# Performance work log

Measured on AMD Instinct MI355X. Metric: run time of the kernel, lower is better.

## Reference

```python
import jax, jax.numpy as jnp
import numpy as np

B, L, HID, NH = 8, 1024, 1024, 16
DH = HID // NH
EPS = 1e-12


def _linear(x, W, b):
    # torch nn.Linear: y = x @ W.T + b
    return jnp.einsum('ble,oe->blo', x, W) + b


def _attend(qx, kx, vx, mask, Wq, bq, Wk, bk, Wv, bv):
    q = _linear(qx, Wq, bq).reshape(B, -1, NH, DH)
    k = _linear(kx, Wk, bk).reshape(B, -1, NH, DH)
    v = _linear(vx, Wv, bv).reshape(B, -1, NH, DH)
    scores = jnp.einsum('bqhd,bkhd->bhqk', q, k) / np.sqrt(DH).astype(np.float32)
    scores = scores + mask  # additive mask broadcast [B,1,1,Lk]
    probs = jax.nn.softmax(scores, axis=-1)  # dropout = identity (eval mode)
    ctx = jnp.einsum('bhqk,bkhd->bqhd', probs, v)
    return ctx.reshape(B, -1, HID)


def _layernorm(x, gamma, beta):
    mu = jnp.mean(x, axis=-1, keepdims=True)
    var = jnp.mean(jnp.square(x - mu), axis=-1, keepdims=True)
    return gamma * (x - mu) * jax.lax.rsqrt(var + EPS) + beta


def setup_inputs():
    key = jax.random.key(0)
    ks = jax.random.split(key, 20)
    s = 0.02
    d = {
        'cinput_tensor': jax.random.normal(ks[0], (B, L, HID), jnp.float32),
        'qinput_tensor': jax.random.normal(ks[1], (B, L, HID), jnp.float32),
        'attention_mask': jnp.zeros((B, 1, 1, L), jnp.float32),
        'qattention_mask': jnp.zeros((B, 1, 1, L), jnp.float32),
    }
    names = ['Wq', 'Wk', 'Wv', 'Wqq', 'Wqk', 'Wqv', 'Wo']
    for i, n in enumerate(names):
        d[n] = jax.random.normal(ks[2 + i], (HID, HID), jnp.float32) * s
        d['b' + n[1:]] = jnp.zeros((HID,), jnp.float32)
    d['gamma'] = jnp.ones((HID,), jnp.float32)
    d['beta'] = jnp.zeros((HID,), jnp.float32)
    return d


def reference(cinput_tensor, qinput_tensor, attention_mask, qattention_mask,
              Wq, bq, Wk, bk, Wv, bv, Wqq, bqq, Wqk, bqk, Wqv, bqv,
              Wo, bo, gamma, beta):
    enc, dec = cinput_tensor, qinput_tensor
    # c-branch: query from dec, key/value from enc
    ctx = _attend(dec, enc, enc, attention_mask, Wq, bq, Wk, bk, Wv, bv)
    # q-branch: query from enc, key/value from dec
    qctx = _attend(enc, dec, dec, qattention_mask, Wqq, bqq, Wqk, bqk, Wqv, bqv)
    # output: same dense/LayerNorm reused, and BOTH residuals add cinput_tensor
    # (faithful to the original module, including its apparent bug)
    c_out = _layernorm(_linear(ctx, Wo, bo) + cinput_tensor, gamma, beta)
    q_out = _layernorm(_linear(qctx, Wo, bo) + cinput_tensor, gamma, beta)
    return (c_out, q_out)
```

## Files before the change

kernel.cpp:

```cpp
#include <hip/hip_runtime.h>

typedef __bf16 bf16;
typedef unsigned short u16;
typedef __bf16 bf16x8 __attribute__((ext_vector_type(8)));
typedef __bf16 bf16x4 __attribute__((ext_vector_type(4)));
typedef float f32x4 __attribute__((ext_vector_type(4)));

#define GLD16(g, l) __builtin_amdgcn_global_load_lds( \
    (const __attribute__((address_space(1))) void*)(g), \
    (__attribute__((address_space(3))) void*)(l), 16, 0, 0)

#define MFMA_BF16 __builtin_amdgcn_mfma_f32_16x16x32_bf16

#define FENCE() asm volatile("" ::: "memory")
#define BARRIER() do { FENCE(); __builtin_amdgcn_s_barrier(); FENCE(); } while (0)

struct CvtFlat { const float* s[9]; bf16* d[9]; int off[10]; };

__global__ __launch_bounds__(256) void cvt_flat(CvtFlat a) {
  const int g = blockIdx.x * 256 + threadIdx.x;
  int seg = 0;
  #pragma unroll
  for (int i = 1; i < 9; ++i) seg += (g >= a.off[i]) ? 1 : 0;
  const int loc = (g - a.off[seg]) * 4;
  const f32x4 v = *(const f32x4*)(a.s[seg] + loc);
  bf16x4 o;
  #pragma unroll
  for (int j = 0; j < 4; ++j) o[j] = (bf16)v[j];
  *(bf16x4*)(a.d[seg] + loc) = o;
}

struct GemmDesc {
  const bf16* X;
  const bf16* W;
  const float* B;
  const float* R;
  bf16* Y;
  int vt;
};
struct GemmArgs { GemmDesc d[6]; };

__device__ __forceinline__ void stage_slice(const bf16* G, int row0, int k0,
                                            u16* slot, int w, int lane) {
  #pragma unroll
  for (int i = 0; i < 2; ++i) {
    const int sb = i * 512 + w * 64;
    const int s = sb + lane;
    const int r = s >> 2, c = (s & 3) ^ ((r >> 1) & 3);
    GLD16(G + (row0 + r) * 1024 + k0 + c * 8, &slot[sb * 8]);
  }
}

template <bool STAGE, int VW>
__device__ __forceinline__ void do_slice(
    int sv, u16 (&As)[4][8192], u16 (&Bs)[4][8192], f32x4 (&acc)[8][4],
    const int (&offA)[8], const int (&offB)[4],
    const bf16* __restrict__ X, const bf16* __restrict__ W,
    int m0, int n0, int w, int lane) {
  const u16* Asl = &As[sv & 3][0];
  const u16* Bsl = &Bs[sv & 3][0];
  bf16x8 a[4], b[4];
  #pragma unroll
  for (int mt = 0; mt < 4; ++mt) a[mt] = *(const bf16x8*)&Asl[offA[mt]];
  #pragma unroll
  for (int nt = 0; nt < 4; ++nt) b[nt] = *(const bf16x8*)&Bsl[offB[nt]];
  if constexpr (STAGE)
    stage_slice(X, m0, (sv + 3) * 32, &As[(sv + 3) & 3][0], w, lane);
  BARRIER();
  asm volatile("s_waitcnt lgkmcnt(0)" ::: "memory");
  __builtin_amdgcn_s_setprio(1);
  #pragma unroll
  for (int mt = 0; mt < 4; ++mt)
    #pragma unroll
    for (int nt = 0; nt < 4; ++nt)
      acc[mt][nt] = MFMA_BF16(a[mt], b[nt], acc[mt][nt], 0, 0, 0);
  __builtin_amdgcn_s_setprio(0);
  BARRIER();
  #pragma unroll
  for (int mt = 0; mt < 4; ++mt) a[mt] = *(const bf16x8*)&Asl[offA[4 + mt]];
  if constexpr (STAGE)
    stage_slice(W, n0, (sv + 3) * 32, &Bs[(sv + 3) & 3][0], w, lane);
  BARRIER();
  asm volatile("s_waitcnt lgkmcnt(0)" ::: "memory");
  __builtin_amdgcn_s_setprio(1);
  #pragma unroll
  for (int mt = 0; mt < 4; ++mt)
    #pragma unroll
    for (int nt = 0; nt < 4; ++nt)
      acc[4 + mt][nt] = MFMA_BF16(a[mt], b[nt], acc[4 + mt][nt], 0, 0, 0);
  __builtin_amdgcn_s_setprio(0);
  if constexpr (VW == 8)      asm volatile("s_waitcnt vmcnt(8)" ::: "memory");
  else if constexpr (VW == 4) asm volatile("s_waitcnt vmcnt(4)" ::: "memory");
  else if constexpr (VW == 0) asm volatile("s_waitcnt vmcnt(0)" ::: "memory");
  BARRIER();
}

__global__ __launch_bounds__(512, 2) void gemm256(GemmArgs args) {
  const GemmDesc g = args.d[blockIdx.z];
  __shared__ u16 As[4][8192];
  __shared__ u16 Bs[4][8192];
  const int tid = threadIdx.x;
  const int w = tid >> 6, lane = tid & 63;
  const int lq = lane >> 4, ll = lane & 15;
  const int wr = w >> 2, wc = w & 3;
  const int lin = blockIdx.x + (blockIdx.y << 3);
  const int tile = (lin & 7) * 16 + (lin >> 3);
  const int mtile = tile >> 2, ntile = tile & 3;
  const int m0 = mtile * 256, n0 = ntile * 256;
  f32x4 acc[8][4] = {};

  int offA[8], offB[4];
  #pragma unroll
  for (int mt = 0; mt < 8; ++mt) {
    const int am = wr * 128 + mt * 16 + ll;
    offA[mt] = (am * 4 + (lq ^ ((am >> 1) & 3))) * 8;
  }
  #pragma unroll
  for (int nt = 0; nt < 4; ++nt) {
    const int bn = wc * 64 + nt * 16 + ll;
    offB[nt] = (bn * 4 + (lq ^ ((bn >> 1) & 3))) * 8;
  }

  #pragma unroll
  for (int ss = 0; ss < 3; ++ss) {
    stage_slice(g.X, m0, ss * 32, &As[ss][0], w, lane);
    stage_slice(g.W, n0, ss * 32, &Bs[ss][0], w, lane);
  }
  asm volatile("s_waitcnt vmcnt(8)" ::: "memory");
  BARRIER();

  #pragma unroll 4
  for (int s = 0; s < 28; ++s)
    do_slice<true, 8>(s, As, Bs, acc, offA, offB, g.X, g.W, m0, n0, w, lane);
  do_slice<true, 8>(28, As, Bs, acc, offA, offB, g.X, g.W, m0, n0, w, lane);
  do_slice<false, 4>(29, As, Bs, acc, offA, offB, g.X, g.W, m0, n0, w, lane);
  do_slice<false, 0>(30, As, Bs, acc, offA, offB, g.X, g.W, m0, n0, w, lane);
  do_slice<false, -1>(31, As, Bs, acc, offA, offB, g.X, g.W, m0, n0, w, lane);

  float biasv[4];
  #pragma unroll
  for (int nt = 0; nt < 4; ++nt) biasv[nt] = g.B[n0 + wc * 64 + nt * 16 + ll];

  #pragma unroll
  for (int mt = 0; mt < 8; ++mt) {
    #pragma unroll
    for (int r = 0; r < 4; ++r) {
      const int m = m0 + wr * 128 + mt * 16 + lq * 4 + r;
      #pragma unroll
      for (int nt = 0; nt < 4; ++nt) {
        const int n = n0 + wc * 64 + nt * 16 + ll;
        float v = acc[mt][nt][r] + biasv[nt];
        if (g.R) v += g.R[m * 1024 + n];
        if (!g.vt) {
          g.Y[m * 1024 + n] = (bf16)v;
        } else {
          const int bb = m >> 10, tok = m & 1023;
          g.Y[(((bb << 4) + (n >> 6)) * 64 + (n & 63)) * 1024 + tok] = (bf16)v;
        }
      }
    }
  }
}

struct AttnDesc { const bf16* Qp; const bf16* Kp; const bf16* Vt; const float* mask; bf16* ctx; };

__global__ __launch_bounds__(256, 4) void attn_kernel(AttnDesc A0, AttnDesc A1) {
  const AttnDesc A = blockIdx.z ? A1 : A0;
  __shared__ u16 Ks[128 * 64];
  __shared__ u16 Vts[64 * 128];
  __shared__ u16 Pts[4 * 1024];
  const int tid = threadIdx.x;
  const int w = tid >> 6, lane = tid & 63;
  const int lq = lane >> 4, ll = lane & 15;
  const int lin = blockIdx.x + (blockIdx.y << 3);
  const int bh = (lin & 7) | ((lin >> 6) << 3);
  const int q0 = ((lin >> 3) & 7) * 128;
  const int b = bh >> 4, h = bh & 15;
  const float* mrow = A.mask + b * 1024;

  #pragma unroll
  for (int i = 0; i < 4; ++i) {
    const int sb = w * 256 + i * 64;
    const int s = sb + lane;
    const int r = s >> 3, c = (s & 7) ^ (r & 7);
    GLD16(A.Qp + (b * 1024 + q0 + r) * 1024 + h * 64 + c * 8, &Ks[sb * 8]);
  }
  __syncthreads();
  bf16x8 bq[2][2];
  #pragma unroll
  for (int nt = 0; nt < 2; ++nt)
    #pragma unroll
    for (int kd = 0; kd < 2; ++kd) {
      const int row = w * 32 + nt * 16 + ll;
      const int c8 = kd * 4 + lq;
      bq[nt][kd] = *(const bf16x8*)&Ks[row * 64 + ((c8 ^ (row & 7)) << 3)];
    }
  __syncthreads();

  f32x4 oacc[4][2] = {};
  float rsum[2] = {0.f, 0.f};

  for (int kt = 0; kt < 8; ++kt) {
    const int kk0 = kt * 128;
    #pragma unroll
    for (int i = 0; i < 4; ++i) {
      const int sb = w * 256 + i * 64;
      const int s = sb + lane;
      { const int r = s >> 3, c = (s & 7) ^ (r & 7);
        GLD16(A.Kp + (b * 1024 + kk0 + r) * 1024 + h * 64 + c * 8, &Ks[sb * 8]); }
      { const int r = s >> 4, c = (s & 15) ^ (r & 15);
        GLD16(A.Vt + (bh * 64 + r) * 1024 + kk0 + c * 8, &Vts[sb * 8]); }
    }
    __syncthreads();

    #pragma unroll
    for (int qtr = 0; qtr < 4; ++qtr) {
      bf16x8 ak[2][2];
      #pragma unroll
      for (int mh = 0; mh < 2; ++mh) {
        const int row = qtr * 32 + mh * 16 + ll;
        #pragma unroll
        for (int kd = 0; kd < 2; ++kd) {
          const int c8 = kd * 4 + lq;
          ak[mh][kd] = *(const bf16x8*)&Ks[row * 64 + ((c8 ^ (row & 7)) << 3)];
        }
      }
      f32x4 sacc[2][2] = {};
      #pragma unroll
      for (int mh = 0; mh < 2; ++mh)
        #pragma unroll
        for (int nt = 0; nt < 2; ++nt)
          #pragma unroll
          for (int kd = 0; kd < 2; ++kd)
            sacc[mh][nt] = MFMA_BF16(ak[mh][kd], bq[nt][kd], sacc[mh][nt], 0, 0, 0);

      f32x4 mv[2];
      #pragma unroll
      for (int mh = 0; mh < 2; ++mh)
        mv[mh] = *(const f32x4*)&mrow[kk0 + qtr * 32 + mh * 16 + lq * 4];

      #pragma unroll
      for (int mh = 0; mh < 2; ++mh)
        #pragma unroll
        for (int nt = 0; nt < 2; ++nt) {
          bf16x4 pv;
          #pragma unroll
          for (int rr = 0; rr < 4; ++rr) {
            const float p = __expf(fmaf(sacc[mh][nt][rr], 0.125f, mv[mh][rr]));
            rsum[nt] += p;
            pv[rr] = (bf16)p;
          }
          const int row = nt * 16 + ll;
          const int gq = mh * 2 + (lq >> 1);
          *(bf16x4*)&Pts[w * 1024 + row * 32 + ((gq ^ (row & 3)) << 3) + (lq & 1) * 4] = pv;
        }

      bf16x8 bp[2];
      #pragma unroll
      for (int nt = 0; nt < 2; ++nt) {
        const int row = nt * 16 + ll;
        bp[nt] = *(const bf16x8*)&Pts[w * 1024 + row * 32 + ((lq ^ (row & 3)) << 3)];
      }
      #pragma unroll
      for (int mtd = 0; mtd < 4; ++mtd) {
        const int row = mtd * 16 + ll;
        const int c16 = (qtr * 4 + lq) ^ (row & 15);
        const bf16x8 av = *(const bf16x8*)&Vts[row * 128 + (c16 << 3)];
        oacc[mtd][0] = MFMA_BF16(av, bp[0], oacc[mtd][0], 0, 0, 0);
        oacc[mtd][1] = MFMA_BF16(av, bp[1], oacc[mtd][1], 0, 0, 0);
      }
    }
    __syncthreads();
  }

  #pragma unroll
  for (int nt = 0; nt < 2; ++nt) {
    rsum[nt] += __shfl_xor(rsum[nt], 16, 64);
    rsum[nt] += __shfl_xor(rsum[nt], 32, 64);
  }

  #pragma unroll
  for (int nt = 0; nt < 2; ++nt) {
    const float inv = 1.f / rsum[nt];
    const int tok = q0 + w * 32 + nt * 16 + ll;
    #pragma unroll
    for (int mtd = 0; mtd < 4; ++mtd) {
      bf16x4 ov;
      #pragma unroll
      for (int rr = 0; rr < 4; ++rr) ov[rr] = (bf16)(oacc[mtd][nt][rr] * inv);
      *(bf16x4*)&A.ctx[(size_t)(b * 1024 + tok) * 1024 + h * 64 + mtd * 16 + lq * 4] = ov;
    }
  }
}

__global__ __launch_bounds__(256) void ln_kernel(const bf16* __restrict__ pre_c,
                                                 const bf16* __restrict__ pre_q,
                                                 const float* __restrict__ gamma,
                                                 const float* __restrict__ beta,
                                                 float* __restrict__ out) {
  const int row = blockIdx.x;
  const bf16* src = (row < 8192) ? (pre_c + (size_t)row * 1024)
                                 : (pre_q + (size_t)(row - 8192) * 1024);
  float* dst = out + (size_t)row * 1024;
  const int t = threadIdx.x;
  const bf16x4 xv = *(const bf16x4*)(src + t * 4);
  float x[4]; float s = 0.f, ss = 0.f;
  #pragma unroll
  for (int i = 0; i < 4; ++i) { x[i] = (float)xv[i]; s += x[i]; ss += x[i] * x[i]; }
  #pragma unroll
  for (int off = 1; off < 64; off <<= 1) { s += __shfl_xor(s, off, 64); ss += __shfl_xor(ss, off, 64); }
  __shared__ float red[8];
  const int w = t >> 6, lane = t & 63;
  if (lane == 0) { red[w * 2] = s; red[w * 2 + 1] = ss; }
  __syncthreads();
  s  = red[0] + red[2] + red[4] + red[6];
  ss = red[1] + red[3] + red[5] + red[7];
  const float mu = s * (1.f / 1024.f);
  float var = ss * (1.f / 1024.f) - mu * mu;
  var = fmaxf(var, 0.f);
  const float rs = rsqrtf(var + 1e-12f);
  const f32x4 gv = *(const f32x4*)(gamma + t * 4);
  const f32x4 bv = *(const f32x4*)(beta + t * 4);
  f32x4 yv;
  #pragma unroll
  for (int i = 0; i < 4; ++i) yv[i] = gv[i] * (x[i] - mu) * rs + bv[i];
  *(f32x4*)(dst + t * 4) = yv;
}

extern "C" void kernel_launch(void* const* d_in, const int* in_sizes, int n_in,
                              void* d_out, int out_size, void* d_ws, size_t ws_size,
                              hipStream_t stream) {
  const float* enc    = (const float*)d_in[0];
  const float* dec    = (const float*)d_in[1];
  const float* mask_c = (const float*)d_in[2];
  const float* mask_q = (const float*)d_in[3];
  const float* Wq  = (const float*)d_in[4];  const float* bq  = (const float*)d_in[5];
  const float* Wk  = (const float*)d_in[6];  const float* bk  = (const float*)d_in[7];
  const float* Wv  = (const float*)d_in[8];  const float* bv  = (const float*)d_in[9];
  const float* Wqq = (const float*)d_in[10]; const float* bqq = (const float*)d_in[11];
  const float* Wqk = (const float*)d_in[12]; const float* bqk = (const float*)d_in[13];
  const float* Wqv = (const float*)d_in[14]; const float* bqv = (const float*)d_in[15];
  const float* Wo  = (const float*)d_in[16]; const float* bo  = (const float*)d_in[17];
  const float* gamma = (const float*)d_in[18];
  const float* beta  = (const float*)d_in[19];
  float* out = (float*)d_out;

  bf16* ws = (bf16*)d_ws;
  const size_t XSZ = (size_t)8192 * 1024;
  const size_t WSZ = (size_t)1024 * 1024;
  bf16* enc_b = ws;
  bf16* dec_b = enc_b + XSZ;
  bf16* Wb[7];
  for (int i = 0; i < 7; ++i) Wb[i] = dec_b + XSZ + i * WSZ;
  bf16* after_w = Wb[6] + WSZ;

  CvtFlat ca;
  ca.s[0] = enc; ca.d[0] = enc_b;
  ca.s[1] = dec; ca.d[1] = dec_b;
  const float* Wsrc[7] = {Wq, Wk, Wv, Wqq, Wqk, Wqv, Wo};
  for (int i = 0; i < 7; ++i) { ca.s[2 + i] = Wsrc[i]; ca.d[2 + i] = Wb[i]; }
  int running = 0;
  const int segn[9] = {(int)(XSZ / 4), (int)(XSZ / 4), (int)(WSZ / 4), (int)(WSZ / 4),
                       (int)(WSZ / 4), (int)(WSZ / 4), (int)(WSZ / 4), (int)(WSZ / 4), (int)(WSZ / 4)};
  for (int i = 0; i < 9; ++i) { ca.off[i] = running; running += segn[i]; }
  ca.off[9] = running;
  const int cvt_blocks = running / 256;

  const size_t need_par = (size_t)(23 + 48) * 1024 * 1024 * 2;

  cvt_flat<<<dim3(cvt_blocks), 256, 0, stream>>>(ca);

  if (ws_size >= need_par) {
    bf16* Qc  = after_w;        bf16* Kc  = Qc + XSZ;  bf16* Vtc = Kc + XSZ;
    bf16* Qq  = Vtc + XSZ;      bf16* Kq  = Qq + XSZ;  bf16* Vtq = Kq + XSZ;
    bf16* ctx_c = enc_b;
    bf16* ctx_q = dec_b;
    bf16* pre_c = Qc;
    bf16* pre_q = Qq;

    GemmArgs pa = {};
    pa.d[0] = {dec_b, Wb[0], bq,  nullptr, Qc,  0};
    pa.d[1] = {enc_b, Wb[1], bk,  nullptr, Kc,  0};
    pa.d[2] = {enc_b, Wb[2], bv,  nullptr, Vtc, 1};
    pa.d[3] = {enc_b, Wb[3], bqq, nullptr, Qq,  0};
    pa.d[4] = {dec_b, Wb[4], bqk, nullptr, Kq,  0};
    pa.d[5] = {dec_b, Wb[5], bqv, nullptr, Vtq, 1};
    gemm256<<<dim3(8, 16, 6), 512, 0, stream>>>(pa);

    AttnDesc a0 = {Qc, Kc, Vtc, mask_c, ctx_c};
    AttnDesc a1 = {Qq, Kq, Vtq, mask_q, ctx_q};
    attn_kernel<<<dim3(8, 128, 2), 256, 0, stream>>>(a0, a1);

    GemmArgs oa = {};
    oa.d[0] = {ctx_c, Wb[6], bo, enc, pre_c, 0};
    oa.d[1] = {ctx_q, Wb[6], bo, enc, pre_q, 0};
    gemm256<<<dim3(8, 16, 2), 512, 0, stream>>>(oa);

    ln_kernel<<<dim3(16384), 256, 0, stream>>>(pre_c, pre_q, gamma, beta, out);
  } else {
    bf16* Q  = after_w;  bf16* K = Q + XSZ;  bf16* Vt = K + XSZ;
    bf16* ctx_c = Vt + XSZ;
    bf16* ctx_q = ctx_c + XSZ;
    bf16* pre_c = Q;
    bf16* pre_q = K;

    GemmArgs pa = {};
    pa.d[0] = {dec_b, Wb[0], bq,  nullptr, Q,  0};
    pa.d[1] = {enc_b, Wb[1], bk,  nullptr, K,  0};
    pa.d[2] = {enc_b, Wb[2], bv,  nullptr, Vt, 1};
    gemm256<<<dim3(8, 16, 3), 512, 0, stream>>>(pa);

    AttnDesc a0 = {Q, K, Vt, mask_c, ctx_c};
    attn_kernel<<<dim3(8, 128, 1), 256, 0, stream>>>(a0, a0);

    GemmArgs pb = {};
    pb.d[0] = {enc_b, Wb[3], bqq, nullptr, Q,  0};
    pb.d[1] = {dec_b, Wb[4], bqk, nullptr, K,  0};
    pb.d[2] = {dec_b, Wb[5], bqv, nullptr, Vt, 1};
    gemm256<<<dim3(8, 16, 3), 512, 0, stream>>>(pb);

    AttnDesc a1 = {Q, K, Vt, mask_q, ctx_q};
    attn_kernel<<<dim3(8, 128, 1), 256, 0, stream>>>(a1, a1);

    GemmArgs oa = {};
    oa.d[0] = {ctx_c, Wb[6], bo, enc, pre_c, 0};
    oa.d[1] = {ctx_q, Wb[6], bo, enc, pre_q, 0};
    gemm256<<<dim3(8, 16, 2), 512, 0, stream>>>(oa);

    ln_kernel<<<dim3(16384), 256, 0, stream>>>(pre_c, pre_q, gamma, beta, out);
  }
}
```

Before: 535.3 us.

## Merge GEMM slice halves into one phase with fewer barriers and precomputed staging offsets

Restructures the per-K-slice loop of the 256x256 GEMM. Previously each slice ran in two halves, each with its own barriers and waits. Now all eight A fragments and four B fragments are loaded up front, the async global-to-LDS loads for slice s+3 are issued, and all 32 MFMAs run in a single block, leaving one barrier per slice. Staging addresses are precomputed once outside the loop. This removes several barriers and lgkmcnt waits per slice and some address arithmetic, at the cost of more VGPRs for fragments (occupancy risk at launch bounds 512,2) and reliance on the 4-buffer ring for correctness without the intermediate barriers.

```diff
diff --git a/kernel.cpp b/kernel.cpp
--- a/kernel.cpp
+++ b/kernel.cpp
@@ -40,54 +40,34 @@
 };
 struct GemmArgs { GemmDesc d[6]; };
 
-__device__ __forceinline__ void stage_slice(const bf16* G, int row0, int k0,
-                                            u16* slot, int w, int lane) {
-  #pragma unroll
-  for (int i = 0; i < 2; ++i) {
-    const int sb = i * 512 + w * 64;
-    const int s = sb + lane;
-    const int r = s >> 2, c = (s & 3) ^ ((r >> 1) & 3);
-    GLD16(G + (row0 + r) * 1024 + k0 + c * 8, &slot[sb * 8]);
-  }
-}
-
 template <bool STAGE, int VW>
 __device__ __forceinline__ void do_slice(
     int sv, u16 (&As)[4][8192], u16 (&Bs)[4][8192], f32x4 (&acc)[8][4],
     const int (&offA)[8], const int (&offB)[4],
     const bf16* __restrict__ X, const bf16* __restrict__ W,
-    int m0, int n0, int w, int lane) {
+    const int (&aoff)[2], const int (&boff)[2], const int (&sdst)[2]) {
   const u16* Asl = &As[sv & 3][0];
   const u16* Bsl = &Bs[sv & 3][0];
-  bf16x8 a[4], b[4];
-  #pragma unroll
-  for (int mt = 0; mt < 4; ++mt) a[mt] = *(const bf16x8*)&Asl[offA[mt]];
+  bf16x8 a[8], b[4];
   #pragma unroll
   for (int nt = 0; nt < 4; ++nt) b[nt] = *(const bf16x8*)&Bsl[offB[nt]];
-  if constexpr (STAGE)
-    stage_slice(X, m0, (sv + 3) * 32, &As[(sv + 3) & 3][0], w, lane);
-  BARRIER();
-  asm volatile("s_waitcnt lgkmcnt(0)" ::: "memory");
+  #pragma unroll
+  for (int mt = 0; mt < 8; ++mt) a[mt] = *(const bf16x8*)&Asl[offA[mt]];
+  if constexpr (STAGE) {
+    const int k0 = (sv + 3) * 32;
+    u16* Ad = &As[(sv + 3) & 3][0];
+    u16* Bd = &Bs[(sv + 3) & 3][0];
+    #pragma unroll
+    for (int i = 0; i < 2; ++i) GLD16(X + aoff[i] + k0, Ad + sdst[i]);
+    #pragma unroll
+    for (int i = 0; i < 2; ++i) GLD16(W + boff[i] + k0, Bd + sdst[i]);
+  }
   __builtin_amdgcn_s_setprio(1);
   #pragma unroll
-  for (int mt = 0; mt < 4; ++mt)
+  for (int mt = 0; mt < 8; ++mt)
     #pragma unroll
     for (int nt = 0; nt < 4; ++nt)
       acc[mt][nt] = MFMA_BF16(a[mt], b[nt], acc[mt][nt], 0, 0, 0);
-  __builtin_amdgcn_s_setprio(0);
-  BARRIER();
-  #pragma unroll
-  for (int mt = 0; mt < 4; ++mt) a[mt] = *(const bf16x8*)&Asl[offA[4 + mt]];
-  if constexpr (STAGE)
-    stage_slice(W, n0, (sv + 3) * 32, &Bs[(sv + 3) & 3][0], w, lane);
-  BARRIER();
-  asm volatile("s_waitcnt lgkmcnt(0)" ::: "memory");
-  __builtin_amdgcn_s_setprio(1);
-  #pragma unroll
-  for (int mt = 0; mt < 4; ++mt)
-    #pragma unroll
-    for (int nt = 0; nt < 4; ++nt)
-      acc[4 + mt][nt] = MFMA_BF16(a[mt], b[nt], acc[4 + mt][nt], 0, 0, 0);
   __builtin_amdgcn_s_setprio(0);
   if constexpr (VW == 8)      asm volatile("s_waitcnt vmcnt(8)" ::: "memory");
   else if constexpr (VW == 4) asm volatile("s_waitcnt vmcnt(4)" ::: "memory");
@@ -121,21 +101,34 @@
     offB[nt] = (bn * 4 + (lq ^ ((bn >> 1) & 3))) * 8;
   }
 
+  int aoff[2], boff[2], sdst[2];
+  #pragma unroll
+  for (int i = 0; i < 2; ++i) {
+    const int sb = i * 512 + w * 64;
+    const int s = sb + lane;
+    const int r = s >> 2, c = (s & 3) ^ ((r >> 1) & 3);
+    aoff[i] = (m0 + r) * 1024 + c * 8;
+    boff[i] = (n0 + r) * 1024 + c * 8;
+    sdst[i] = sb * 8;
+  }
+
   #pragma unroll
   for (int ss = 0; ss < 3; ++ss) {
-    stage_slice(g.X, m0, ss * 32, &As[ss][0], w, lane);
-    stage_slice(g.W, n0, ss * 32, &Bs[ss][0], w, lane);
+    const int k0 = ss * 32;
+    #pragma unroll
+    for (int i = 0; i < 2; ++i) GLD16(g.X + aoff[i] + k0, &As[ss][sdst[i]]);
+    #pragma unroll
+    for (int i = 0; i < 2; ++i) GLD16(g.W + boff[i] + k0, &Bs[ss][sdst[i]]);
   }
   asm volatile("s_waitcnt vmcnt(8)" ::: "memory");
   BARRIER();
 
   #pragma unroll 4
-  for (int s = 0; s < 28; ++s)
-    do_slice<true, 8>(s, As, Bs, acc, offA, offB, g.X, g.W, m0, n0, w, lane);
-  do_slice<true, 8>(28, As, Bs, acc, offA, offB, g.X, g.W, m0, n0, w, lane);
-  do_slice<false, 4>(29, As, Bs, acc, offA, offB, g.X, g.W, m0, n0, w, lane);
-  do_slice<false, 0>(30, As, Bs, acc, offA, offB, g.X, g.W, m0, n0, w, lane);
-  do_slice<false, -1>(31, As, Bs, acc, offA, offB, g.X, g.W, m0, n0, w, lane);
+  for (int s = 0; s < 29; ++s)
+    do_slice<true, 8>(s, As, Bs, acc, offA, offB, g.X, g.W, aoff, boff, sdst);
+  do_slice<false, 4>(29, As, Bs, acc, offA, offB, g.X, g.W, aoff, boff, sdst);
+  do_slice<false, 0>(30, As, Bs, acc, offA, offB, g.X, g.W, aoff, boff, sdst);
+  do_slice<false, -1>(31, As, Bs, acc, offA, offB, g.X, g.W, aoff, boff, sdst);
 
   float biasv[4];
   #pragma unroll
```

After: 498.7 us. 1.07x faster.
